# Optimization experiments

Measured on AMD Instinct MI355X. Metric: run time of the kernel, lower is better.

Reference implementation:

```python
import jax, jax.numpy as jnp
import numpy as np

EPS = 1e-20

def _conv(x, w, pad):
    return jax.lax.conv_general_dilated(
        x, w, (1, 1), [(pad, pad), (pad, pad)],
        dimension_numbers=('NCHW', 'OIHW', 'NCHW'))

def _nconv(x, c, w_raw, b, pad):
    # Normalized convolution with SoftPlus-enforced positive weights.
    w = jax.nn.softplus(w_raw)
    denom = _conv(c, w, pad)
    nomin = _conv(x * c, w, pad)
    out = nomin / (denom + EPS) + b[None, :, None, None]
    s = jnp.sum(w.reshape(w.shape[0], -1), axis=-1)  # per-out-channel kernel sum
    cout = denom / s[None, :, None, None]
    return out, cout

def _pool_gather(x, c):
    # max_pool2d(c, 2, 2, return_indices=True), then gather x at those indices.
    B, C, H, W = c.shape
    win = lambda t: t.reshape(B, C, H // 2, 2, W // 2, 2).transpose(0, 1, 2, 4, 3, 5).reshape(B, C, H // 2, W // 2, 4)
    cw, xw = win(c), win(x)
    idx = jnp.argmax(cw, axis=-1)
    take = lambda t: jnp.take_along_axis(t, idx[..., None], axis=-1)[..., 0]
    return take(xw), take(cw) / 4.0  # c1_ds /= 4

def _up2(t):
    return jnp.repeat(jnp.repeat(t, 2, axis=2), 2, axis=3)

def setup_inputs() -> dict:
    key = jax.random.key(0)
    ks = jax.random.split(key, 16)
    B, H, W, C = 8, 352, 1216, 8
    inp = {
        'x0': jax.random.normal(ks[0], (B, 1, H, W), jnp.float32),
        'c0': jax.random.uniform(ks[1], (B, 1, H, W), jnp.float32),
        'w1': jax.random.normal(ks[2], (C, 1, 5, 5), jnp.float32) * 0.1,
        'b1': jax.random.normal(ks[3], (C,), jnp.float32) * 0.01,
        'w2': jax.random.normal(ks[4], (C, C, 5, 5), jnp.float32) * 0.1,
        'b2': jax.random.normal(ks[5], (C,), jnp.float32) * 0.01,
        'w3': jax.random.normal(ks[6], (C, C, 5, 5), jnp.float32) * 0.1,
        'b3': jax.random.normal(ks[7], (C,), jnp.float32) * 0.01,
        'w4': jax.random.normal(ks[8], (C, 2 * C, 3, 3), jnp.float32) * 0.1,
        'b4': jax.random.normal(ks[9], (C,), jnp.float32) * 0.01,
        'w5': jax.random.normal(ks[10], (C, 2 * C, 3, 3), jnp.float32) * 0.1,
        'b5': jax.random.normal(ks[11], (C,), jnp.float32) * 0.01,
        'w6': jax.random.normal(ks[12], (C, 2 * C, 3, 3), jnp.float32) * 0.1,
        'b6': jax.random.normal(ks[13], (C,), jnp.float32) * 0.01,
        'w7': jax.random.normal(ks[14], (1, C, 1, 1), jnp.float32) * 0.1,
        'b7': jax.random.normal(ks[15], (1,), jnp.float32) * 0.01,
    }
    return inp

def reference(x0, c0, w1, b1, w2, b2, w3, b3, w4, b4, w5, b5, w6, b6, w7, b7):
    x1, c1 = _nconv(x0, c0, w1, b1, 2)
    x1, c1 = _nconv(x1, c1, w2, b2, 2)
    x1, c1 = _nconv(x1, c1, w3, b3, 2)
    # downsample 1 (confidence-guided unpool indices)
    x1_ds, c1_ds = _pool_gather(x1, c1)
    x2_ds, c2_ds = _nconv(x1_ds, c1_ds, w2, b2, 2)   # nconv2 reused
    x2_ds, c2_ds = _nconv(x2_ds, c2_ds, w3, b3, 2)   # nconv3 reused
    # downsample 2
    x2_dss, c2_dss = _pool_gather(x2_ds, c2_ds)
    x3_ds, c3_ds = _nconv(x2_dss, c2_dss, w2, b2, 2)
    # downsample 3
    x3_dss, c3_dss = _pool_gather(x3_ds, c3_ds)
    x4_ds, c4_ds = _nconv(x3_dss, c3_dss, w2, b2, 2)
    # decoder with nearest upsample + concat + nconv
    x4, c4 = _up2(x4_ds), _up2(c4_ds)
    x34_ds, c34_ds = _nconv(jnp.concatenate((x3_ds, x4), 1), jnp.concatenate((c3_ds, c4), 1), w4, b4, 1)
    x34, c34 = _up2(x34_ds), _up2(c34_ds)
    x23_ds, c23_ds = _nconv(jnp.concatenate((x2_ds, x34), 1), jnp.concatenate((c2_ds, c34), 1), w5, b5, 1)
    x23, c23 = _up2(x23_ds), _up2(c23_ds)
    xout, cout = _nconv(jnp.concatenate((x23, x1), 1), jnp.concatenate((c23, c1), 1), w6, b6, 1)
    xout, cout = _nconv(xout, cout, w7, b7, 0)
    return xout, cout
```

## Files before the change

kernel.cpp:

```cpp
#include <hip/hip_runtime.h>
#include <cmath>

#define EPSV 1e-20f
#define MFMA16(A, B, C) __builtin_amdgcn_mfma_f32_16x16x32_f16(A, B, C, 0, 0, 0)

typedef _Float16 f16;
typedef _Float16 v8h __attribute__((ext_vector_type(8)));
typedef _Float16 h4 __attribute__((ext_vector_type(4)));
typedef float v4f __attribute__((ext_vector_type(4)));
typedef float f32x2 __attribute__((ext_vector_type(2)));

__device__ __forceinline__ float softplusf(float x) {
    return fmaxf(x, 0.f) + log1pf(expf(-fabsf(x)));
}

__device__ __forceinline__ v8h v8h_zero() {
    v8h z = {0, 0, 0, 0, 0, 0, 0, 0};
    return z;
}

__global__ void prep_scalars(const float* __restrict__ w1, const float* __restrict__ w2,
                             const float* __restrict__ w3, const float* __restrict__ w4,
                             const float* __restrict__ w5, const float* __restrict__ w6,
                             const float* __restrict__ w7, float* __restrict__ WT) {
    __shared__ float lds[1600];
    const float* srcs[7] = {w1, w2, w3, w4, w5, w6, w7};
    const int ns[7]    = {200, 1600, 1600, 1152, 1152, 1152, 8};
    const int pers[7]  = {25, 200, 200, 144, 144, 144, 8};
    const int couts[7] = {8, 8, 8, 8, 8, 8, 1};
    int t = blockIdx.x;
    const float* src = srcs[t];
    int n = ns[t];
    for (int i = threadIdx.x; i < n; i += blockDim.x) {
        float v = softplusf(src[i]);
        lds[i] = v;
        if (t == 0) WT[i] = v;
        if (t == 6) WT[256 + i] = v;
    }
    __syncthreads();
    if ((int)threadIdx.x < couts[t]) {
        float s = 0.f;
        int per = pers[t];
        for (int i = 0; i < per; ++i) s += lds[threadIdx.x * per + i];
        WT[200 + t * 8 + threadIdx.x] = s;
    }
}

__global__ void pack_enc_frag(const float* __restrict__ w2, const float* __restrict__ w3,
                              f16* __restrict__ dst2, f16* __restrict__ dst3) {
    const float* w = blockIdx.x ? w3 : w2;
    f16* dst = blockIdx.x ? dst3 : dst2;
    for (int i = threadIdx.x; i < 7 * 64 * 8; i += blockDim.x) {
        int g = i >> 9;
        int l = (i >> 3) & 63;
        int j = i & 7;
        int co = l & 15, sub = l >> 4;
        float v = 0.f;
        if (co < 8) {
            int kh = 0, kw = 0;
            bool valid = true;
            if (g < 5) { kh = g; kw = sub; }
            else if (g == 5) { kh = sub; kw = 4; }
            else { kh = 4; kw = 4; valid = (sub == 0); }
            if (valid) v = softplusf(w[((co * 8 + j) * 5 + kh) * 5 + kw]);
        }
        dst[i] = (f16)v;
    }
}

__global__ void pack_dec_frag(const float* __restrict__ w4, const float* __restrict__ w5,
                              const float* __restrict__ w6,
                              f16* __restrict__ dst4, f16* __restrict__ dst5,
                              f16* __restrict__ dst6) {
    const float* ww[3] = {w4, w5, w6};
    f16* dd[3] = {dst4, dst5, dst6};
    const int RBt[3] = {0, 0, 1};
    const float* w = ww[blockIdx.x];
    f16* dst = dd[blockIdx.x];
    const int rb = RBt[blockIdx.x], sbk = 1 - rb;
    for (int i = threadIdx.x; i < 7 * 64 * 8; i += blockDim.x) {
        int g = i >> 9;
        int l = (i >> 3) & 63;
        int j = i & 7;
        int co = l & 15, sub = l >> 4;
        float v = 0.f;
        if (co < 8 && sub < 3) {
            int kw = sub;
            auto W_ = [&](int blk, int kh) {
                return softplusf(w[((co * 16 + blk * 8 + j) * 3 + kh) * 3 + kw]);
            };
            if (g < 3) v = W_(rb, g);
            else if (g == 3) v = W_(sbk, 0);
            else if (g == 4) v = W_(sbk, 1) + W_(sbk, 2);
            else if (g == 5) v = W_(sbk, 0) + W_(sbk, 1);
            else v = W_(sbk, 2);
        }
        dst[i] = (f16)v;
    }
}

__device__ __forceinline__ void load_row8_f(const float* __restrict__ row, int c0, int W,
                                            float v[8]) {
    if (c0 >= 0 && c0 + 8 <= W) {
#pragma unroll
        for (int i = 0; i < 4; ++i) {
            f32x2 t = *(const f32x2*)(row + c0 + 2 * i);
            v[2 * i] = t[0];
            v[2 * i + 1] = t[1];
        }
    } else {
#pragma unroll
        for (int i = 0; i < 8; ++i) {
            int c = c0 + i;
            v[i] = (c >= 0 && c < W) ? row[c] : 0.f;
        }
    }
}

__global__ void __launch_bounds__(256) nconv_l1(
    const float* __restrict__ x0, const float* __restrict__ c0,
    const float* __restrict__ wp, const float* __restrict__ ssum,
    const float* __restrict__ bias,
    f16* __restrict__ xcout, f16* __restrict__ cout,
    int B, int H, int W) {
    __shared__ __attribute__((aligned(16))) float wl[200];
    for (int i = threadIdx.x; i < 200; i += 256) {
        int co = i & 7, r = i >> 3;
        wl[i] = wp[co * 25 + r];
    }
    __syncthreads();

    const int Wq = W >> 2;
    int idx = blockIdx.x * 256 + threadIdx.x;
    int total = B * H * Wq;
    if (idx >= total) return;
    int w0 = (idx % Wq) << 2;
    int h = (idx / Wq) % H;
    int b = idx / (Wq * H);
    const int HW = H * W;

    float den[4][8] = {}, nom[4][8] = {};
    const float* cp = c0 + (size_t)b * HW;
    const float* xp = x0 + (size_t)b * HW;

    for (int kh = 0; kh < 5; ++kh) {
        int ih = h + kh - 2;
        if (ih < 0 || ih >= H) continue;
        float cv[8], xr[8], xv[8];
        load_row8_f(cp + (size_t)ih * W, w0 - 2, W, cv);
        load_row8_f(xp + (size_t)ih * W, w0 - 2, W, xr);
#pragma unroll
        for (int i = 0; i < 8; ++i) xv[i] = xr[i] * cv[i];
        const float* wrow = &wl[kh * 5 * 8];
#pragma unroll
        for (int kw = 0; kw < 5; ++kw) {
            const float4* wq = (const float4*)&wrow[kw * 8];
            float4 wa = wq[0], wb = wq[1];
            float wv[8] = {wa.x, wa.y, wa.z, wa.w, wb.x, wb.y, wb.z, wb.w};
#pragma unroll
            for (int co = 0; co < 8; ++co)
#pragma unroll
                for (int p = 0; p < 4; ++p) {
                    den[p][co] = fmaf(wv[co], cv[p + kw], den[p][co]);
                    nom[p][co] = fmaf(wv[co], xv[p + kw], nom[p][co]);
                }
        }
    }

    float rssv[8], bbv[8];
#pragma unroll
    for (int co = 0; co < 8; ++co) {
        rssv[co] = __builtin_amdgcn_rcpf(ssum[co]);
        bbv[co] = bias[co];
    }
    unsigned pa = (unsigned)(((b * H + h) * W + w0) * 8);
#pragma unroll
    for (int p = 0; p < 4; ++p) {
        v8h xc8, c8;
#pragma unroll
        for (int co = 0; co < 8; ++co) {
            float d = den[p][co];
            float cc = d * rssv[co];
            float xo = nom[p][co] * __builtin_amdgcn_rcpf(d + EPSV) + bbv[co];
            xc8[co] = (f16)(xo * cc);
            c8[co] = (f16)cc;
        }
        *(v8h*)(xcout + pa + p * 8) = xc8;
        *(v8h*)(cout + pa + p * 8) = c8;
    }
}

__global__ void __launch_bounds__(256) pool_nhwc(
    const f16* __restrict__ xc, const f16* __restrict__ c,
    f16* __restrict__ xo, f16* __restrict__ co_,
    int B, int H, int W) {
    int H2 = H >> 1, W2 = W >> 1, Wh = W2 >> 1;
    int idx = blockIdx.x * 256 + threadIdx.x;
    int total = B * H2 * Wh;
    if (idx >= total) return;
    int wo = (idx % Wh) * 2;
    int ho = (idx / Wh) % H2;
    int b = idx / (Wh * H2);
    unsigned base = (unsigned)(((b * H + 2 * ho) * W + 2 * wo) * 8);
    unsigned rb = (unsigned)(W * 8);
    v8h c0r[4], c1r[4], x0r[4], x1r[4];
#pragma unroll
    for (int i = 0; i < 4; ++i) {
        c0r[i] = *(const v8h*)(c + base + 8 * i);
        c1r[i] = *(const v8h*)(c + base + rb + 8 * i);
        x0r[i] = *(const v8h*)(xc + base + 8 * i);
        x1r[i] = *(const v8h*)(xc + base + rb + 8 * i);
    }
    unsigned oa = (unsigned)(((b * H2 + ho) * W2 + wo) * 8);
#pragma unroll
    for (int p = 0; p < 2; ++p) {
        v8h xr, cr;
#pragma unroll
        for (int e = 0; e < 8; ++e) {
            float b0 = (float)c0r[2 * p][e], b1 = (float)c0r[2 * p + 1][e];
            float b2 = (float)c1r[2 * p][e], b3 = (float)c1r[2 * p + 1][e];
            float cb = b0;
            float xv = (float)x0r[2 * p][e];
            if (b1 > cb) { cb = b1; xv = (float)x0r[2 * p + 1][e]; }
            if (b2 > cb) { cb = b2; xv = (float)x1r[2 * p][e]; }
            if (b3 > cb) { cb = b3; xv = (float)x1r[2 * p + 1][e]; }
            xr[e] = (f16)(xv * 0.25f);
            cr[e] = (f16)(cb * 0.25f);
        }
        *(v8h*)(xo + oa + p * 8) = xr;
        *(v8h*)(co_ + oa + p * 8) = cr;
    }
}

__global__ void __launch_bounds__(256) enc5_mfma(
    const f16* __restrict__ xcin, const f16* __restrict__ cin,
    const f16* __restrict__ bfrag, const float* __restrict__ ssum,
    const float* __restrict__ bias,
    f16* __restrict__ xcout, f16* __restrict__ cout,
    int B, int H, int W, int CH) {
    const int lane = threadIdx.x & 63;
    const int wid = threadIdx.x >> 6;
    const int m = lane & 15, sub = lane >> 4;
    const int tilesW = (W + 15) >> 4;
    const int tw = blockIdx.x * 4 + wid;
    if (tw >= tilesW) return;
    const int w0 = tw << 4;
    const int b = blockIdx.z;
    const int h0 = blockIdx.y * CH;

    v8h bf[7];
#pragma unroll
    for (int g = 0; g < 7; ++g)
        bf[g] = *(const v8h*)(bfrag + ((g << 6) + lane) * 8);

    float4 ssv = {1.f, 1.f, 1.f, 1.f}, bbv = {0.f, 0.f, 0.f, 0.f};
    if (sub < 2) {
        ssv = *(const float4*)(ssum + sub * 4);
        bbv = *(const float4*)(bias + sub * 4);
    }
    float rssv[4];
#pragma unroll
    for (int j = 0; j < 4; ++j) rssv[j] = __builtin_amdgcn_rcpf(((const float*)&ssv)[j]);

    const unsigned W8u = (unsigned)W * 8;
    const unsigned bb8 = (unsigned)(b * H) * W8u;
    unsigned sbase = bb8 + (unsigned)h0 * W8u + (unsigned)(w0 + m) * 8 + sub * 4;

    auto epi = [&](const v4f& accd, const v4f& accn, unsigned sb) {
        h4 xo8, c8;
#pragma unroll
        for (int j = 0; j < 4; ++j) {
            float d = accd[j];
            float cc = d * rssv[j];
            float x = accn[j] * __builtin_amdgcn_rcpf(d + EPSV) + ((const float*)&bbv)[j];
            c8[j] = (f16)cc;
            xo8[j] = (f16)(x * cc);
        }
        *(h4*)(cout + sb) = c8;
        *(h4*)(xcout + sb) = xo8;
    };

    const bool fast = (w0 >= 2) && (w0 + 17 < W) && (h0 >= 2) && (h0 + CH + 2 <= H);
    if (fast) {
        v8h Rc[5], Rx[5];
        unsigned aRot = bb8 + (unsigned)(h0 - 2) * W8u + (unsigned)(w0 + m + sub - 2) * 8;
#pragma unroll
        for (int t = 0; t < 4; ++t) {
            Rc[t] = *(const v8h*)(cin + aRot);
            Rx[t] = *(const v8h*)(xcin + aRot);
            aRot += W8u;
        }
        unsigned aE5 = bb8 + (unsigned)(h0 + sub - 2) * W8u + (unsigned)(w0 + m + 2) * 8;
        unsigned aE6 = bb8 + (unsigned)(h0 + 2) * W8u + (unsigned)(w0 + m + 2) * 8;
        const bool st = (sub < 2);
        for (int hh = 0; hh < CH; hh += 5) {
#pragma unroll
            for (int p = 0; p < 5; ++p) {
                Rc[(p + 4) % 5] = *(const v8h*)(cin + aRot);
                Rx[(p + 4) % 5] = *(const v8h*)(xcin + aRot);
                aRot += W8u;
                v8h e5c = *(const v8h*)(cin + aE5);
                v8h e5x = *(const v8h*)(xcin + aE5);
                aE5 += W8u;
                v8h e6c = *(const v8h*)(cin + aE6);
                v8h e6x = *(const v8h*)(xcin + aE6);
                aE6 += W8u;

                v4f accd = {0.f, 0.f, 0.f, 0.f}, accn = {0.f, 0.f, 0.f, 0.f};
#pragma unroll
                for (int g = 0; g < 5; ++g) {
                    accd = MFMA16(bf[g], Rc[(p + g) % 5], accd);
                    accn = MFMA16(bf[g], Rx[(p + g) % 5], accn);
                }
                accd = MFMA16(bf[5], e5c, accd);
                accn = MFMA16(bf[5], e5x, accn);
                accd = MFMA16(bf[6], e6c, accd);
                accn = MFMA16(bf[6], e6x, accn);

                if (st) epi(accd, accn, sbase);
                sbase += W8u;
            }
        }
    } else {
        const int cwr = w0 + m + sub - 2;
        const bool okc_r = (cwr >= 0) && (cwr < W);
        const unsigned a_rot = (unsigned)min(max(cwr, 0), W - 1) * 8;
        const int cwe = w0 + m + 2;
        const bool okc_e = cwe < W;
        const unsigned a_e = (unsigned)min(cwe, W - 1) * 8;
        const bool doStore = (sub < 2) && (w0 + m < W);

        v8h Rc[5], Rx[5];
#pragma unroll
        for (int t = 0; t < 4; ++t) {
            int r = h0 - 2 + t;
            bool ok = (r >= 0) && (r < H) && okc_r;
            unsigned a = bb8 + (unsigned)min(max(r, 0), H - 1) * W8u + a_rot;
            v8h pc = *(const v8h*)(cin + a);
            v8h px = *(const v8h*)(xcin + a);
            Rc[t] = ok ? pc : v8h_zero();
            Rx[t] = ok ? px : v8h_zero();
        }
        Rc[4] = v8h_zero();
        Rx[4] = v8h_zero();

        for (int hh = 0; hh < CH; hh += 5) {
#pragma unroll
            for (int p = 0; p < 5; ++p) {
                const int h = h0 + hh + p;
                {
                    int r = h + 2;
                    bool ok = (r < H) && okc_r;
                    unsigned a = bb8 + (unsigned)min(r, H - 1) * W8u + a_rot;
                    v8h pc = *(const v8h*)(cin + a);
                    v8h px = *(const v8h*)(xcin + a);
                    Rc[(p + 4) % 5] = ok ? pc : v8h_zero();
                    Rx[(p + 4) % 5] = ok ? px : v8h_zero();
                }
                v8h e5c, e5x;
                {
                    int r = h + sub - 2;
                    bool ok = (r >= 0) && (r < H) && okc_e;
                    unsigned a = bb8 + (unsigned)min(max(r, 0), H - 1) * W8u + a_e;
                    v8h pc = *(const v8h*)(cin + a);
                    v8h px = *(const v8h*)(xcin + a);
                    e5c = ok ? pc : v8h_zero();
                    e5x = ok ? px : v8h_zero();
                }
                v8h e6c, e6x;
                {
                    int r = h + 2;
                    bool ok = (r < H) && okc_e;
                    unsigned a = bb8 + (unsigned)min(r, H - 1) * W8u + a_e;
                    v8h pc = *(const v8h*)(cin + a);
                    v8h px = *(const v8h*)(xcin + a);
                    e6c = ok ? pc : v8h_zero();
                    e6x = ok ? px : v8h_zero();
                }

                v4f accd = {0.f, 0.f, 0.f, 0.f}, accn = {0.f, 0.f, 0.f, 0.f};
#pragma unroll
                for (int g = 0; g < 5; ++g) {
                    accd = MFMA16(bf[g], Rc[(p + g) % 5], accd);
                    accn = MFMA16(bf[g], Rx[(p + g) % 5], accn);
                }
                accd = MFMA16(bf[5], e5c, accd);
                accn = MFMA16(bf[5], e5x, accn);
                accd = MFMA16(bf[6], e6c, accd);
                accn = MFMA16(bf[6], e6x, accn);

                if (doStore && h < H) epi(accd, accn, sbase);
                sbase += W8u;
            }
        }
    }
}

template <bool FUSE7>
__global__ void __launch_bounds__(256) dec3_mfma(
    const f16* __restrict__ xcR, const f16* __restrict__ cR,
    const f16* __restrict__ xcS, const f16* __restrict__ cS,
    const f16* __restrict__ bfrag,
    const float* __restrict__ ssum, const float* __restrict__ bias,
    const float* __restrict__ wp7, const float* __restrict__ s7p,
    const float* __restrict__ b7p,
    f16* __restrict__ xcout, f16* __restrict__ ccout,
    float* __restrict__ xoutf, float* __restrict__ coutf,
    int B, int H, int W, int CH) {
    const int lane = threadIdx.x & 63;
    const int wid = threadIdx.x >> 6;
    const int m = lane & 15, sub = lane >> 4;
    const int tilesW = W >> 4;
    const int tw = blockIdx.x * 4 + wid;
    if (tw >= tilesW) return;
    const int w0 = tw << 4;
    const int b = blockIdx.z;
    const int h0 = blockIdx.y * CH;

    v8h bf[7];
#pragma unroll
    for (int g = 0; g < 7; ++g)
        bf[g] = *(const v8h*)(bfrag + ((g << 6) + lane) * 8);

    const int cw = w0 + m + sub - 1;
    const bool okc = (cw >= 0) && (cw < W);
    const int cwc = min(max(cw, 0), W - 1);
    const unsigned aRc = (unsigned)cwc * 8;
    const unsigned aSc = (unsigned)(cwc >> 1) * 8;

    const int Hs = H >> 1, Ws = W >> 1;
    const unsigned WR8 = (unsigned)W * 8;
    const unsigned WS8 = (unsigned)Ws * 8;
    const unsigned bbR = (unsigned)(b * H) * WR8;
    const unsigned bbS = (unsigned)(b * Hs) * WS8;

    float4 ssv = {1.f, 1.f, 1.f, 1.f}, bbv = {0.f, 0.f, 0.f, 0.f};
    float4 w7v = {0.f, 0.f, 0.f, 0.f};
    if (sub < 2) {
        ssv = *(const float4*)(ssum + sub * 4);
        bbv = *(const float4*)(bias + sub * 4);
        if (FUSE7) w7v = *(const float4*)(wp7 + sub * 4);
    }
    float rssv[4];
#pragma unroll
    for (int j = 0; j < 4; ++j) rssv[j] = __builtin_amdgcn_rcpf(((const float*)&ssv)[j]);
    float rs7 = 0.f, b7v = 0.f;
    if (FUSE7) { rs7 = __builtin_amdgcn_rcpf(s7p[0]); b7v = b7p[0]; }

    unsigned sbase = bbR + (unsigned)h0 * WR8 + (unsigned)(w0 + m) * 8 + sub * 4;
    unsigned opix = (unsigned)(b * H + h0) * (unsigned)W + (unsigned)w0;

    auto epi = [&](const v4f& accd, const v4f& accn) {
        if constexpr (FUSE7) {
            float td = 0.f, tn = 0.f;
#pragma unroll
            for (int j = 0; j < 4; ++j) {
                float d = accd[j];
                float cc = d * rssv[j];
                float o = accn[j] * __builtin_amdgcn_rcpf(d + EPSV) + ((const float*)&bbv)[j];
                td = fmaf(((const float*)&w7v)[j], cc, td);
                tn = fmaf(((const float*)&w7v)[j], o * cc, tn);
            }
            td += __shfl_xor(td, 16);
            tn += __shfl_xor(tn, 16);
            td += __shfl_xor(td, 32);
            tn += __shfl_xor(tn, 32);
            if (sub == 0) {
                xoutf[opix + m] = tn * __builtin_amdgcn_rcpf(td + EPSV) + b7v;
            } else if (sub == 1) {
                coutf[opix + m] = td * rs7;
            }
        } else {
            if (sub < 2) {
                h4 xo8, c8;
#pragma unroll
                for (int j = 0; j < 4; ++j) {
                    float d = accd[j];
                    float cc = d * rssv[j];
                    float x = accn[j] * __builtin_amdgcn_rcpf(d + EPSV) + ((const float*)&bbv)[j];
                    c8[j] = (f16)cc;
                    xo8[j] = (f16)(x * cc);
                }
                *(h4*)(ccout + sbase) = c8;
                *(h4*)(xcout + sbase) = xo8;
            }
        }
    };

    const bool fast = (w0 >= 1) && (w0 + 17 < W) && (h0 >= 2) && (h0 + CH + 1 <= H);
    if (fast) {
        v8h Rc_[3], Rx_[3], Sc_[3], Sx_[3];
        unsigned ar = bbR + (unsigned)(h0 - 1) * WR8 + aRc;
        Rc_[2] = *(const v8h*)(cR + ar); Rx_[2] = *(const v8h*)(xcR + ar); ar += WR8;
        Rc_[0] = *(const v8h*)(cR + ar); Rx_[0] = *(const v8h*)(xcR + ar); ar += WR8;
        const int k0 = h0 >> 1;
        unsigned as_ = bbS + (unsigned)(k0 - 1) * WS8 + aSc;
        Sc_[2] = *(const v8h*)(cS + as_); Sx_[2] = *(const v8h*)(xcS + as_); as_ += WS8;
        Sc_[0] = *(const v8h*)(cS + as_); Sx_[0] = *(const v8h*)(xcS + as_); as_ += WS8;

        for (int hh = 0; hh < CH; hh += 6) {
#pragma unroll
            for (int p = 0; p < 6; ++p) {
                const int j = p >> 1;
                Rc_[(p + 1) % 3] = *(const v8h*)(cR + ar);
                Rx_[(p + 1) % 3] = *(const v8h*)(xcR + ar);
                ar += WR8;
                if ((p & 1) == 0) {
                    Sc_[(j + 1) % 3] = *(const v8h*)(cS + as_);
                    Sx_[(j + 1) % 3] = *(const v8h*)(xcS + as_);
                    as_ += WS8;
                }
                v4f accd = {0.f, 0.f, 0.f, 0.f}, accn = {0.f, 0.f, 0.f, 0.f};
#pragma unroll
                for (int g = 0; g < 3; ++g) {
                    accd = MFMA16(bf[g], Rc_[(p + g + 2) % 3], accd);
                    accn = MFMA16(bf[g], Rx_[(p + g + 2) % 3], accn);
                }
                if ((p & 1) == 0) {
                    accd = MFMA16(bf[3], Sc_[(j + 2) % 3], accd);
                    accn = MFMA16(bf[3], Sx_[(j + 2) % 3], accn);
                    accd = MFMA16(bf[4], Sc_[j % 3], accd);
                    accn = MFMA16(bf[4], Sx_[j % 3], accn);
                } else {
                    accd = MFMA16(bf[5], Sc_[j % 3], accd);
                    accn = MFMA16(bf[5], Sx_[j % 3], accn);
                    accd = MFMA16(bf[6], Sc_[(j + 1) % 3], accd);
                    accn = MFMA16(bf[6], Sx_[(j + 1) % 3], accn);
                }
                epi(accd, accn);
                sbase += WR8;
                opix += W;
            }
        }
    } else {
        for (int hh = 0; hh < CH; ++hh) {
            const int h = h0 + hh;
            if (h >= H) break;
            const int k = h >> 1;
            const bool ev = (h & 1) == 0;
            v4f accd = {0.f, 0.f, 0.f, 0.f}, accn = {0.f, 0.f, 0.f, 0.f};
#pragma unroll
            for (int g = 0; g < 3; ++g) {
                int r = h + g - 1;
                bool ok = okc && (r >= 0) && (r < H);
                unsigned a = bbR + (unsigned)min(max(r, 0), H - 1) * WR8 + aRc;
                v8h pc = *(const v8h*)(cR + a);
                v8h px = *(const v8h*)(xcR + a);
                if (!ok) { pc = v8h_zero(); px = v8h_zero(); }
                accd = MFMA16(bf[g], pc, accd);
                accn = MFMA16(bf[g], px, accn);
            }
            {
                int rs = ev ? (k - 1) : k;
                bool ok = okc && (!ev || (h >= 1));
                unsigned a = bbS + (unsigned)min(max(rs, 0), Hs - 1) * WS8 + aSc;
                v8h pc = *(const v8h*)(cS + a);
                v8h px = *(const v8h*)(xcS + a);
                if (!ok) { pc = v8h_zero(); px = v8h_zero(); }
                v8h wA = ev ? bf[3] : bf[5];
                accd = MFMA16(wA, pc, accd);
                accn = MFMA16(wA, px, accn);
            }
            {
                int rs = ev ? k : (k + 1);
                bool ok = okc && (ev || (h + 1 < H));
                unsigned a = bbS + (unsigned)min(max(rs, 0), Hs - 1) * WS8 + aSc;
                v8h pc = *(const v8h*)(cS + a);
                v8h px = *(const v8h*)(xcS + a);
                if (!ok) { pc = v8h_zero(); px = v8h_zero(); }
                v8h wB = ev ? bf[4] : bf[6];
                accd = MFMA16(wB, pc, accd);
                accn = MFMA16(wB, px, accn);
            }
            epi(accd, accn);
            sbase += WR8;
            opix += W;
        }
    }
}

extern "C" void kernel_launch(void* const* d_in, const int* in_sizes, int n_in,
                              void* d_out, int out_size, void* d_ws, size_t ws_size,
                              hipStream_t stream) {
    const float* x0 = (const float*)d_in[0];
    const float* c0 = (const float*)d_in[1];
    const float* w1 = (const float*)d_in[2];
    const float* b1 = (const float*)d_in[3];
    const float* w2 = (const float*)d_in[4];
    const float* b2 = (const float*)d_in[5];
    const float* w3 = (const float*)d_in[6];
    const float* b3 = (const float*)d_in[7];
    const float* w4 = (const float*)d_in[8];
    const float* b4 = (const float*)d_in[9];
    const float* w5 = (const float*)d_in[10];
    const float* b5 = (const float*)d_in[11];
    const float* w6 = (const float*)d_in[12];
    const float* b6 = (const float*)d_in[13];
    const float* w7 = (const float*)d_in[14];
    const float* b7 = (const float*)d_in[15];

    const int B = 8, H = 352, W = 1216;
    const int H2 = 176, W2 = 608, H4 = 88, W4 = 304, H8 = 44, W8 = 152;
    const size_t F   = (size_t)64 * H * W;
    const size_t H2s = (size_t)64 * H2 * W2;
    const size_t Qs  = (size_t)64 * H4 * W4;
    const size_t Es  = (size_t)64 * H8 * W8;

    const size_t needH = 4 * F * sizeof(f16) + 7168 * sizeof(float);
    if (ws_size < needH) return;

    f16* ws = (f16*)d_ws;
    f16* P0x = ws;
    f16* P0c = ws + F;
    f16* Ux  = ws + 2 * F;
    f16* Uc  = ws + 3 * F;
    f16* D1x = ws + 2 * F;
    f16* D1c = D1x + H2s;
    f16* D2x = D1c + H2s;
    f16* D2c = D2x + H2s;
    f16* Q1x = ws + 3 * F;
    f16* Q1c = Q1x + Qs;
    f16* Q2x = Q1c + Qs;
    f16* Q2c = Q2x + Qs;
    f16* E1x = Q2c + Qs;
    f16* E1c = E1x + Es;
    f16* E2x = E1c + Es;
    f16* E2c = E2x + Es;
    f16* DF4 = ws + 3 * F + 16777216;
    f16* DF5 = DF4 + 3584;
    f16* DF6 = DF5 + 3584;

    char* tail = (char*)d_ws + 4 * F * sizeof(f16);
    float* WT = (float*)tail;
    f16* BF2 = (f16*)(tail + 2048);
    f16* BF3 = (f16*)(tail + 9216);

    const float* s1 = WT + 200;
    const float* s2 = WT + 208;
    const float* s3 = WT + 216;
    const float* s4 = WT + 224;
    const float* s5 = WT + 232;
    const float* s6 = WT + 240;
    const float* s7 = WT + 248;
    const float* wp7 = WT + 256;

    prep_scalars<<<7, 256, 0, stream>>>(w1, w2, w3, w4, w5, w6, w7, WT);
    pack_enc_frag<<<2, 256, 0, stream>>>(w2, w3, BF2, BF3);

    auto nb = [](size_t n) { return (int)((n + 255) / 256); };
    const dim3 geF(19, 18, 8);
    const dim3 geH(10, 9, 8);
    const dim3 geQ(5, 9, 8);
    const dim3 geE(3, 9, 8);
    const dim3 gdF(19, 30, 8);
    const dim3 gdH(10, 15, 8);
    const dim3 gdQ(5, 8, 8);

    nconv_l1<<<nb((size_t)B * H * (W / 4)), 256, 0, stream>>>(
        x0, c0, WT, s1, b1, P0x, P0c, B, H, W);
    enc5_mfma<<<geF, 256, 0, stream>>>(P0x, P0c, BF2, s2, b2, Ux, Uc, B, H, W, 20);
    enc5_mfma<<<geF, 256, 0, stream>>>(Ux, Uc, BF3, s3, b3, P0x, P0c, B, H, W, 20);
    pack_dec_frag<<<3, 256, 0, stream>>>(w4, w5, w6, DF4, DF5, DF6);
    pool_nhwc<<<nb((size_t)B * H2 * (W2 / 2)), 256, 0, stream>>>(P0x, P0c, D1x, D1c, B, H, W);
    enc5_mfma<<<geH, 256, 0, stream>>>(D1x, D1c, BF2, s2, b2, D2x, D2c, B, H2, W2, 20);
    enc5_mfma<<<geH, 256, 0, stream>>>(D2x, D2c, BF3, s3, b3, D1x, D1c, B, H2, W2, 20);
    pool_nhwc<<<nb((size_t)B * H4 * (W4 / 2)), 256, 0, stream>>>(D1x, D1c, Q1x, Q1c, B, H2, W2);
    enc5_mfma<<<geQ, 256, 0, stream>>>(Q1x, Q1c, BF2, s2, b2, Q2x, Q2c, B, H4, W4, 10);
    pool_nhwc<<<nb((size_t)B * H8 * (W8 / 2)), 256, 0, stream>>>(Q2x, Q2c, E1x, E1c, B, H4, W4);
    enc5_mfma<<<geE, 256, 0, stream>>>(E1x, E1c, BF2, s2, b2, E2x, E2c, B, H8, W8, 5);

    dec3_mfma<false><<<gdQ, 256, 0, stream>>>(
        Q2x, Q2c, E2x, E2c, DF4, s4, b4, WT, WT, WT,
        Q1x, Q1c, (float*)nullptr, (float*)nullptr, B, H4, W4, 12);
    dec3_mfma<false><<<gdH, 256, 0, stream>>>(
        D1x, D1c, Q1x, Q1c, DF5, s5, b5, WT, WT, WT,
        D2x, D2c, (float*)nullptr, (float*)nullptr, B, H2, W2, 12);

    float* outx = (float*)d_out;
    float* outc = outx + (size_t)B * H * W;
    dec3_mfma<true><<<gdF, 256, 0, stream>>>(
        P0x, P0c, D2x, D2c, DF6, s6, b6, wp7, s7, b7,
        (f16*)nullptr, (f16*)nullptr, outx, outc, B, H, W, 12);
}
```

Baseline: 426.1 us.

## Compute first nconv layer with MFMA and merge weight prep kernels

Replaces the scalar-FMA first layer (1-channel 5x5 normalized conv) with an MFMA kernel. The 25 taps are packed into a 16x32 f16 fragment, and each lane streams rows of input through a rolling register window. The two prep kernels are merged into one launch that also packs the layer-1 fragment. When the workspace is large enough, the decoder weight packing moves to the start. The layer-1 inputs and weights are now rounded to fp16, which reduces accuracy, and MFMA lanes are partly wasted because only 8 of 16 output rows are used.

```diff
diff --git a/kernel.cpp b/kernel.cpp
--- a/kernel.cpp
+++ b/kernel.cpp
@@ -8,7 +8,6 @@
 typedef _Float16 v8h __attribute__((ext_vector_type(8)));
 typedef _Float16 h4 __attribute__((ext_vector_type(4)));
 typedef float v4f __attribute__((ext_vector_type(4)));
-typedef float f32x2 __attribute__((ext_vector_type(2)));
 
 __device__ __forceinline__ float softplusf(float x) {
     return fmaxf(x, 0.f) + log1pf(expf(-fabsf(x)));
@@ -19,52 +18,64 @@
     return z;
 }
 
-__global__ void prep_scalars(const float* __restrict__ w1, const float* __restrict__ w2,
-                             const float* __restrict__ w3, const float* __restrict__ w4,
-                             const float* __restrict__ w5, const float* __restrict__ w6,
-                             const float* __restrict__ w7, float* __restrict__ WT) {
-    __shared__ float lds[1600];
-    const float* srcs[7] = {w1, w2, w3, w4, w5, w6, w7};
-    const int ns[7]    = {200, 1600, 1600, 1152, 1152, 1152, 8};
-    const int pers[7]  = {25, 200, 200, 144, 144, 144, 8};
-    const int couts[7] = {8, 8, 8, 8, 8, 8, 1};
+__global__ void prep_misc(const float* __restrict__ w1, const float* __restrict__ w2,
+                          const float* __restrict__ w3, const float* __restrict__ w4,
+                          const float* __restrict__ w5, const float* __restrict__ w6,
+                          const float* __restrict__ w7, float* __restrict__ WT,
+                          f16* __restrict__ BF2, f16* __restrict__ BF3,
+                          f16* __restrict__ BF1) {
     int t = blockIdx.x;
-    const float* src = srcs[t];
-    int n = ns[t];
-    for (int i = threadIdx.x; i < n; i += blockDim.x) {
-        float v = softplusf(src[i]);
-        lds[i] = v;
-        if (t == 0) WT[i] = v;
-        if (t == 6) WT[256 + i] = v;
-    }
-    __syncthreads();
-    if ((int)threadIdx.x < couts[t]) {
-        float s = 0.f;
-        int per = pers[t];
-        for (int i = 0; i < per; ++i) s += lds[threadIdx.x * per + i];
-        WT[200 + t * 8 + threadIdx.x] = s;
-    }
-}
-
-__global__ void pack_enc_frag(const float* __restrict__ w2, const float* __restrict__ w3,
-                              f16* __restrict__ dst2, f16* __restrict__ dst3) {
-    const float* w = blockIdx.x ? w3 : w2;
-    f16* dst = blockIdx.x ? dst3 : dst2;
-    for (int i = threadIdx.x; i < 7 * 64 * 8; i += blockDim.x) {
-        int g = i >> 9;
-        int l = (i >> 3) & 63;
-        int j = i & 7;
-        int co = l & 15, sub = l >> 4;
-        float v = 0.f;
-        if (co < 8) {
-            int kh = 0, kw = 0;
-            bool valid = true;
-            if (g < 5) { kh = g; kw = sub; }
-            else if (g == 5) { kh = sub; kw = 4; }
-            else { kh = 4; kw = 4; valid = (sub == 0); }
-            if (valid) v = softplusf(w[((co * 8 + j) * 5 + kh) * 5 + kw]);
-        }
-        dst[i] = (f16)v;
+    if (t < 7) {
+        __shared__ float lds[1600];
+        const float* srcs[7] = {w1, w2, w3, w4, w5, w6, w7};
+        const int ns[7]    = {200, 1600, 1600, 1152, 1152, 1152, 8};
+        const int pers[7]  = {25, 200, 200, 144, 144, 144, 8};
+        const int couts[7] = {8, 8, 8, 8, 8, 8, 1};
+        const float* src = srcs[t];
+        int n = ns[t];
+        for (int i = threadIdx.x; i < n; i += blockDim.x) {
+            float v = softplusf(src[i]);
+            lds[i] = v;
+            if (t == 6) WT[256 + i] = v;
+        }
+        __syncthreads();
+        if ((int)threadIdx.x < couts[t]) {
+            float s = 0.f;
+            int per = pers[t];
+            for (int i = 0; i < per; ++i) s += lds[threadIdx.x * per + i];
+            WT[200 + t * 8 + threadIdx.x] = s;
+        }
+    } else if (t < 9) {
+        const float* w = (t == 8) ? w3 : w2;
+        f16* dst = (t == 8) ? BF3 : BF2;
+        for (int i = threadIdx.x; i < 7 * 64 * 8; i += blockDim.x) {
+            int g = i >> 9;
+            int l = (i >> 3) & 63;
+            int j = i & 7;
+            int co = l & 15, sub = l >> 4;
+            float v = 0.f;
+            if (co < 8) {
+                int kh = 0, kw = 0;
+                bool valid = true;
+                if (g < 5) { kh = g; kw = sub; }
+                else if (g == 5) { kh = sub; kw = 4; }
+                else { kh = 4; kw = 4; valid = (sub == 0); }
+                if (valid) v = softplusf(w[((co * 8 + j) * 5 + kh) * 5 + kw]);
+            }
+            dst[i] = (f16)v;
+        }
+    } else {
+        for (int i = threadIdx.x; i < 512; i += blockDim.x) {
+            int l = i >> 3, j = i & 7;
+            int co = l & 15, sub = l >> 4;
+            float v = 0.f;
+            if (co < 8) {
+                if (j <= 4) v = softplusf(w1[co * 25 + j * 5 + sub]);
+                else if (j == 5) v = softplusf(w1[co * 25 + sub * 5 + 4]);
+                else if (j == 6 && sub == 0) v = softplusf(w1[co * 25 + 24]);
+            }
+            BF1[i] = (f16)v;
+        }
     }
 }
 
@@ -99,94 +110,148 @@
     }
 }
 
-__device__ __forceinline__ void load_row8_f(const float* __restrict__ row, int c0, int W,
-                                            float v[8]) {
-    if (c0 >= 0 && c0 + 8 <= W) {
-#pragma unroll
-        for (int i = 0; i < 4; ++i) {
-            f32x2 t = *(const f32x2*)(row + c0 + 2 * i);
-            v[2 * i] = t[0];
-            v[2 * i + 1] = t[1];
-        }
-    } else {
-#pragma unroll
-        for (int i = 0; i < 8; ++i) {
-            int c = c0 + i;
-            v[i] = (c >= 0 && c < W) ? row[c] : 0.f;
-        }
-    }
-}
-
-__global__ void __launch_bounds__(256) nconv_l1(
+__global__ void __launch_bounds__(256) l1_mfma(
     const float* __restrict__ x0, const float* __restrict__ c0,
-    const float* __restrict__ wp, const float* __restrict__ ssum,
+    const f16* __restrict__ afrag, const float* __restrict__ ssum,
     const float* __restrict__ bias,
     f16* __restrict__ xcout, f16* __restrict__ cout,
-    int B, int H, int W) {
-    __shared__ __attribute__((aligned(16))) float wl[200];
-    for (int i = threadIdx.x; i < 200; i += 256) {
-        int co = i & 7, r = i >> 3;
-        wl[i] = wp[co * 25 + r];
-    }
-    __syncthreads();
-
-    const int Wq = W >> 2;
-    int idx = blockIdx.x * 256 + threadIdx.x;
-    int total = B * H * Wq;
-    if (idx >= total) return;
-    int w0 = (idx % Wq) << 2;
-    int h = (idx / Wq) % H;
-    int b = idx / (Wq * H);
+    int B, int H, int W, int CH) {
+    const int lane = threadIdx.x & 63;
+    const int wid = threadIdx.x >> 6;
+    const int m = lane & 15, sub = lane >> 4;
+    const int tilesW = (W + 15) >> 4;
+    const int tw = blockIdx.x * 4 + wid;
+    if (tw >= tilesW) return;
+    const int w0 = tw << 4;
+    const int b = blockIdx.z;
+    const int h0 = blockIdx.y * CH;
+    if (h0 >= H) return;
+
+    v8h af = *(const v8h*)(afrag + lane * 8);
+
+    float4 ssv = {1.f, 1.f, 1.f, 1.f}, bbv = {0.f, 0.f, 0.f, 0.f};
+    if (sub < 2) {
+        ssv = *(const float4*)(ssum + sub * 4);
+        bbv = *(const float4*)(bias + sub * 4);
+    }
+    float rssv[4];
+#pragma unroll
+    for (int j = 0; j < 4; ++j) rssv[j] = __builtin_amdgcn_rcpf(((const float*)&ssv)[j]);
+
     const int HW = H * W;
-
-    float den[4][8] = {}, nom[4][8] = {};
-    const float* cp = c0 + (size_t)b * HW;
-    const float* xp = x0 + (size_t)b * HW;
-
-    for (int kh = 0; kh < 5; ++kh) {
-        int ih = h + kh - 2;
-        if (ih < 0 || ih >= H) continue;
-        float cv[8], xr[8], xv[8];
-        load_row8_f(cp + (size_t)ih * W, w0 - 2, W, cv);
-        load_row8_f(xp + (size_t)ih * W, w0 - 2, W, xr);
-#pragma unroll
-        for (int i = 0; i < 8; ++i) xv[i] = xr[i] * cv[i];
-        const float* wrow = &wl[kh * 5 * 8];
-#pragma unroll
-        for (int kw = 0; kw < 5; ++kw) {
-            const float4* wq = (const float4*)&wrow[kw * 8];
-            float4 wa = wq[0], wb = wq[1];
-            float wv[8] = {wa.x, wa.y, wa.z, wa.w, wb.x, wb.y, wb.z, wb.w};
-#pragma unroll
-            for (int co = 0; co < 8; ++co)
-#pragma unroll
-                for (int p = 0; p < 4; ++p) {
-                    den[p][co] = fmaf(wv[co], cv[p + kw], den[p][co]);
-                    nom[p][co] = fmaf(wv[co], xv[p + kw], nom[p][co]);
-                }
-        }
-    }
-
-    float rssv[8], bbv[8];
-#pragma unroll
-    for (int co = 0; co < 8; ++co) {
-        rssv[co] = __builtin_amdgcn_rcpf(ssum[co]);
-        bbv[co] = bias[co];
-    }
-    unsigned pa = (unsigned)(((b * H + h) * W + w0) * 8);
-#pragma unroll
-    for (int p = 0; p < 4; ++p) {
-        v8h xc8, c8;
-#pragma unroll
-        for (int co = 0; co < 8; ++co) {
-            float d = den[p][co];
-            float cc = d * rssv[co];
-            float xo = nom[p][co] * __builtin_amdgcn_rcpf(d + EPSV) + bbv[co];
-            xc8[co] = (f16)(xo * cc);
-            c8[co] = (f16)cc;
-        }
-        *(v8h*)(xcout + pa + p * 8) = xc8;
-        *(v8h*)(cout + pa + p * 8) = c8;
+    const float* cb = c0 + (size_t)b * HW;
+    const float* xb = x0 + (size_t)b * HW;
+
+    const unsigned W8u = (unsigned)W * 8;
+    const unsigned bb8 = (unsigned)(b * H) * W8u;
+    unsigned sbase = bb8 + (unsigned)h0 * W8u + (unsigned)(w0 + m) * 8 + sub * 4;
+
+    auto epi = [&](const v4f& accd, const v4f& accn) {
+        h4 xo8, c8;
+#pragma unroll
+        for (int j = 0; j < 4; ++j) {
+            float d = accd[j];
+            float cc = d * rssv[j];
+            float x = accn[j] * __builtin_amdgcn_rcpf(d + EPSV) + ((const float*)&bbv)[j];
+            c8[j] = (f16)cc;
+            xo8[j] = (f16)(x * cc);
+        }
+        *(h4*)(cout + sbase) = c8;
+        *(h4*)(xcout + sbase) = xo8;
+    };
+
+    const int colr = w0 + m + sub - 2;
+    const int cole = w0 + m + 2;
+
+    const bool fast = (w0 >= 2) && (w0 + 17 < W) && (h0 >= 2) && (h0 + CH + 2 <= H);
+    if (fast) {
+        const float* crow = cb + (size_t)(h0 - 2) * W + colr;
+        const float* xrow = xb + (size_t)(h0 - 2) * W + colr;
+        f16 rc[5], rx[5];
+#pragma unroll
+        for (int t = 0; t < 4; ++t) {
+            float cv = *crow, xv = *xrow;
+            crow += W; xrow += W;
+            rc[t] = (f16)cv;
+            rx[t] = (f16)(xv * cv);
+        }
+        rc[4] = (f16)0; rx[4] = (f16)0;
+        const float* c5p = cb + (size_t)(h0 + sub - 2) * W + cole;
+        const float* x5p = xb + (size_t)(h0 + sub - 2) * W + cole;
+        const float* c6p = cb + (size_t)(h0 + 2) * W + cole;
+        const float* x6p = xb + (size_t)(h0 + 2) * W + cole;
+        const bool st = (sub < 2);
+        for (int hh = 0; hh < CH; hh += 5) {
+#pragma unroll
+            for (int p = 0; p < 5; ++p) {
+                float cv = *crow, xv = *xrow;
+                crow += W; xrow += W;
+                rc[(p + 4) % 5] = (f16)cv;
+                rx[(p + 4) % 5] = (f16)(xv * cv);
+                float c5 = *c5p, x5 = *x5p;
+                c5p += W; x5p += W;
+                float c6 = *c6p, x6 = *x6p;
+                c6p += W; x6p += W;
+                f16 e5c = (f16)c5, e5x = (f16)(x5 * c5);
+                f16 e6c = (f16)c6, e6x = (f16)(x6 * c6);
+                v8h bc = {rc[p % 5], rc[(p + 1) % 5], rc[(p + 2) % 5],
+                          rc[(p + 3) % 5], rc[(p + 4) % 5], e5c, e6c, (f16)0};
+                v8h bx = {rx[p % 5], rx[(p + 1) % 5], rx[(p + 2) % 5],
+                          rx[(p + 3) % 5], rx[(p + 4) % 5], e5x, e6x, (f16)0};
+                v4f z = {0.f, 0.f, 0.f, 0.f};
+                v4f accd = MFMA16(af, bc, z);
+                v4f accn = MFMA16(af, bx, z);
+                if (st) epi(accd, accn);
+                sbase += W8u;
+            }
+        }
+    } else {
+        const bool okr = (colr >= 0) && (colr < W);
+        const bool oke = (cole < W);
+        const int colrc = min(max(colr, 0), W - 1);
+        const int colec = min(cole, W - 1);
+        const bool st = (sub < 2) && (w0 + m < W);
+        for (int hh = 0; hh < CH; ++hh) {
+            const int h = h0 + hh;
+            if (h >= H) break;
+            f16 vc[8], vx[8];
+#pragma unroll
+            for (int j = 0; j < 5; ++j) {
+                int r = h + j - 2;
+                bool ok = okr && (r >= 0) && (r < H);
+                int rcl = min(max(r, 0), H - 1);
+                float cv = cb[(size_t)rcl * W + colrc];
+                float xv = xb[(size_t)rcl * W + colrc];
+                vc[j] = ok ? (f16)cv : (f16)0;
+                vx[j] = ok ? (f16)(xv * cv) : (f16)0;
+            }
+            {
+                int r = h + sub - 2;
+                bool ok = oke && (r >= 0) && (r < H);
+                int rcl = min(max(r, 0), H - 1);
+                float cv = cb[(size_t)rcl * W + colec];
+                float xv = xb[(size_t)rcl * W + colec];
+                vc[5] = ok ? (f16)cv : (f16)0;
+                vx[5] = ok ? (f16)(xv * cv) : (f16)0;
+            }
+            {
+                int r = h + 2;
+                bool ok = oke && (r < H);
+                int rcl = min(r, H - 1);
+                float cv = cb[(size_t)rcl * W + colec];
+                float xv = xb[(size_t)rcl * W + colec];
+                vc[6] = ok ? (f16)cv : (f16)0;
+                vx[6] = ok ? (f16)(xv * cv) : (f16)0;
+            }
+            vc[7] = (f16)0; vx[7] = (f16)0;
+            v8h bc = {vc[0], vc[1], vc[2], vc[3], vc[4], vc[5], vc[6], vc[7]};
+            v8h bx = {vx[0], vx[1], vx[2], vx[3], vx[4], vx[5], vx[6], vx[7]};
+            v4f z = {0.f, 0.f, 0.f, 0.f};
+            v4f accd = MFMA16(af, bc, z);
+            v4f accn = MFMA16(af, bx, z);
+            if (st) epi(accd, accn);
+            sbase += W8u;
+        }
     }
 }
 
@@ -247,6 +312,7 @@
     const int w0 = tw << 4;
     const int b = blockIdx.z;
     const int h0 = blockIdx.y * CH;
+    if (h0 >= H) return;
 
     v8h bf[7];
 #pragma unroll
@@ -266,7 +332,7 @@
     const unsigned bb8 = (unsigned)(b * H) * W8u;
     unsigned sbase = bb8 + (unsigned)h0 * W8u + (unsigned)(w0 + m) * 8 + sub * 4;
 
-    auto epi = [&](const v4f& accd, const v4f& accn, unsigned sb) {
+    auto epi = [&](const v4f& accd, const v4f& accn) {
         h4 xo8, c8;
 #pragma unroll
         for (int j = 0; j < 4; ++j) {
@@ -276,8 +342,8 @@
             c8[j] = (f16)cc;
             xo8[j] = (f16)(x * cc);
         }
-        *(h4*)(cout + sb) = c8;
-        *(h4*)(xcout + sb) = xo8;
+        *(h4*)(cout + sbase) = c8;
+        *(h4*)(xcout + sbase) = xo8;
     };
 
     const bool fast = (w0 >= 2) && (w0 + 17 < W) && (h0 >= 2) && (h0 + CH + 2 <= H);
@@ -317,7 +383,7 @@
                 accd = MFMA16(bf[6], e6c, accd);
                 accn = MFMA16(bf[6], e6x, accn);
 
-                if (st) epi(accd, accn, sbase);
+                if (st) epi(accd, accn);
                 sbase += W8u;
             }
         }
@@ -389,7 +455,7 @@
                 accd = MFMA16(bf[6], e6c, accd);
                 accn = MFMA16(bf[6], e6x, accn);
 
-                if (doStore && h < H) epi(accd, accn, sbase);
+                if (doStore && h < H) epi(accd, accn);
                 sbase += W8u;
             }
         }
@@ -416,6 +482,7 @@
     const int w0 = tw << 4;
     const int b = blockIdx.z;
     const int h0 = blockIdx.y * CH;
+    if (h0 >= H) return;
 
     v8h bf[7];
 #pragma unroll
@@ -606,8 +673,10 @@
     const size_t Qs  = (size_t)64 * H4 * W4;
     const size_t Es  = (size_t)64 * H8 * W8;
 
-    const size_t needH = 4 * F * sizeof(f16) + 7168 * sizeof(float);
+    const size_t needH = 4 * F * sizeof(f16) + 28672;
+    const size_t needFull = 4 * F * sizeof(f16) + 65536;
     if (ws_size < needH) return;
+    const bool FULL = (ws_size >= needFull);
 
     f16* ws = (f16*)d_ws;
     f16* P0x = ws;
@@ -626,14 +695,15 @@
     f16* E1c = E1x + Es;
     f16* E2x = E1c + Es;
     f16* E2c = E2x + Es;
-    f16* DF4 = ws + 3 * F + 16777216;
-    f16* DF5 = DF4 + 3584;
-    f16* DF6 = DF5 + 3584;
 
     char* tail = (char*)d_ws + 4 * F * sizeof(f16);
     float* WT = (float*)tail;
     f16* BF2 = (f16*)(tail + 2048);
     f16* BF3 = (f16*)(tail + 9216);
+    f16* BF1 = (f16*)(tail + 16384);
+    f16* DF4 = FULL ? (f16*)(tail + 17408) : (ws + 3 * F + 16777216);
+    f16* DF5 = DF4 + 3584;
+    f16* DF6 = DF5 + 3584;
 
     const float* s1 = WT + 200;
     const float* s2 = WT + 208;
@@ -644,8 +714,9 @@
     const float* s7 = WT + 248;
     const float* wp7 = WT + 256;
 
-    prep_scalars<<<7, 256, 0, stream>>>(w1, w2, w3, w4, w5, w6, w7, WT);
-    pack_enc_frag<<<2, 256, 0, stream>>>(w2, w3, BF2, BF3);
+    prep_misc<<<10, 256, 0, stream>>>(w1, w2, w3, w4, w5, w6, w7, WT, BF2, BF3, BF1);
+    if (FULL)
+        pack_dec_frag<<<3, 256, 0, stream>>>(w4, w5, w6, DF4, DF5, DF6);
 
     auto nb = [](size_t n) { return (int)((n + 255) / 256); };
     const dim3 geF(19, 18, 8);
@@ -656,11 +727,11 @@
     const dim3 gdH(10, 15, 8);
     const dim3 gdQ(5, 8, 8);
 
-    nconv_l1<<<nb((size_t)B * H * (W / 4)), 256, 0, stream>>>(
-        x0, c0, WT, s1, b1, P0x, P0c, B, H, W);
+    l1_mfma<<<geF, 256, 0, stream>>>(x0, c0, BF1, s1, b1, P0x, P0c, B, H, W, 20);
     enc5_mfma<<<geF, 256, 0, stream>>>(P0x, P0c, BF2, s2, b2, Ux, Uc, B, H, W, 20);
     enc5_mfma<<<geF, 256, 0, stream>>>(Ux, Uc, BF3, s3, b3, P0x, P0c, B, H, W, 20);
-    pack_dec_frag<<<3, 256, 0, stream>>>(w4, w5, w6, DF4, DF5, DF6);
+    if (!FULL)
+        pack_dec_frag<<<3, 256, 0, stream>>>(w4, w5, w6, DF4, DF5, DF6);
     pool_nhwc<<<nb((size_t)B * H2 * (W2 / 2)), 256, 0, stream>>>(P0x, P0c, D1x, D1c, B, H, W);
     enc5_mfma<<<geH, 256, 0, stream>>>(D1x, D1c, BF2, s2, b2, D2x, D2c, B, H2, W2, 20);
     enc5_mfma<<<geH, 256, 0, stream>>>(D2x, D2c, BF3, s3, b3, D1x, D1c, B, H2, W2, 20);
```

Result: faster. 414.7 us (-2.7%).
